# Performance work log

Measured on AMD Instinct MI355X. Metric: run time of the kernel, lower is better.

Reference implementation:

```python
import jax, jax.numpy as jnp
import numpy as np

B = 4096
N_DENSE = 13
N_SPARSE = 26
FEAT_PER_SPARSE = 1000
FIELD_NUM = N_DENSE + N_SPARSE          # 39
FEATURE_NUM = N_DENSE + N_SPARSE * FEAT_PER_SPARSE  # 26013
K = 16


def setup_inputs() -> dict:
    key = jax.random.key(0)
    k1, k2, k3, k4 = jax.random.split(key, 4)
    dense_inputs = jax.random.normal(k1, (B, N_DENSE), dtype=jnp.float32)
    sparse_inputs = jax.random.randint(k2, (B, N_SPARSE), 0, FEAT_PER_SPARSE, dtype=jnp.int32)
    w0 = jnp.zeros((1,), dtype=jnp.float32)
    w = jax.random.normal(k3, (FEATURE_NUM, 1), dtype=jnp.float32) * 0.05
    v = jax.random.normal(k4, (FEATURE_NUM, FIELD_NUM, K), dtype=jnp.float32) * 0.05
    return {"dense_inputs": dense_inputs, "sparse_inputs": sparse_inputs,
            "w0": w0, "w": w, "v": v}


def reference(dense_inputs, sparse_inputs, w0, w, v):
    # Feature-index layout matches tf.concat([dense cols, one_hot(sparse_0), ...]):
    # rows [0, N_DENSE) of w/v belong to dense fields, then FEAT_PER_SPARSE rows per sparse field.
    offsets = N_DENSE + FEAT_PER_SPARSE * jnp.arange(N_SPARSE, dtype=sparse_inputs.dtype)
    idx = sparse_inputs + offsets[None, :]               # [B, n_sparse] global feature ids

    # First order: w0 + onehot_concat @ w  ==  w0 + dense part + gathered sparse rows
    first_order = (w0
                   + dense_inputs @ w[:N_DENSE]                       # [B, 1]
                   + jnp.sum(w[idx, 0], axis=1, keepdims=True))       # [B, 1]

    # field_f = tensordot(onehot_concat, v) -> [B, field_num, k]
    field_f = (jnp.einsum('bd,dfk->bfk', dense_inputs, v[:N_DENSE])
               + jnp.sum(v[idx], axis=1))                             # [B, F, K]

    # sum_{i<j} <f_i, f_j> = 0.5 * (||sum_i f_i||^2 - sum_i ||f_i||^2)  (FM identity)
    s = jnp.sum(field_f, axis=1)                                      # [B, K]
    second_order = 0.5 * (jnp.sum(s * s, axis=-1)
                          - jnp.sum(field_f * field_f, axis=(1, 2)))  # [B]
    return first_order + second_order[:, None]
```

## Files before the change

### kernel.cpp

```cpp
#include <hip/hip_runtime.h>

#define NDENSE 13
#define NSPARSE 26
#define FIELD_NUM 39
#define KDIM 16
#define ROW_F4 156
#define BATCH 4096

__global__ __launch_bounds__(256) void ffm_kernel(
    const float* __restrict__ dense,
    const int*   __restrict__ sparse,
    const float* __restrict__ w0,
    const float* __restrict__ w,
    const float4* __restrict__ v4,
    float* __restrict__ out)
{
    const int wave = threadIdx.x >> 6;
    const int lane = threadIdx.x & 63;
    const int b = blockIdx.x * 4 + wave;

    float dv[NDENSE];
#pragma unroll
    for (int d = 0; d < NDENSE; ++d) dv[d] = dense[b * NDENSE + d];

    int myidx = 0;
    if (lane < NSPARSE) {
        myidx = sparse[b * NSPARSE + lane] + NDENSE + 1000 * lane;
    }

    float4 s = make_float4(0.f, 0.f, 0.f, 0.f);
    float  sq = 0.f;

#pragma unroll
    for (int p = 0; p < 3; ++p) {
        const int e4 = lane + 64 * p;
        if (e4 < ROW_F4) {
            float4 acc = make_float4(0.f, 0.f, 0.f, 0.f);
#pragma unroll
            for (int d = 0; d < NDENSE; ++d) {
                const float4 vv = v4[d * ROW_F4 + e4];
                acc.x += dv[d] * vv.x; acc.y += dv[d] * vv.y;
                acc.z += dv[d] * vv.z; acc.w += dv[d] * vv.w;
            }
#pragma unroll
            for (int j = 0; j < NSPARSE; ++j) {
                const int ij = __shfl(myidx, j);
                const float4 vv = v4[ij * ROW_F4 + e4];
                acc.x += vv.x; acc.y += vv.y; acc.z += vv.z; acc.w += vv.w;
            }
            s.x += acc.x; s.y += acc.y; s.z += acc.z; s.w += acc.w;
            sq  += acc.x * acc.x + acc.y * acc.y + acc.z * acc.z + acc.w * acc.w;
        }
    }

#pragma unroll
    for (int m = 4; m <= 32; m <<= 1) {
        s.x += __shfl_xor(s.x, m);
        s.y += __shfl_xor(s.y, m);
        s.z += __shfl_xor(s.z, m);
        s.w += __shfl_xor(s.w, m);
    }
    float s2 = s.x * s.x + s.y * s.y + s.z * s.z + s.w * s.w;
    s2 += __shfl_xor(s2, 1);
    s2 += __shfl_xor(s2, 2);

#pragma unroll
    for (int m = 1; m <= 32; m <<= 1) sq += __shfl_xor(sq, m);

    float fo = 0.f;
    if (lane < NSPARSE) fo = w[myidx];
    if (lane < NDENSE)  fo += dense[b * NDENSE + lane] * w[lane];
#pragma unroll
    for (int m = 1; m <= 32; m <<= 1) fo += __shfl_xor(fo, m);

    if (lane == 0) {
        out[b] = w0[0] + fo + 0.5f * (s2 - sq);
    }
}

extern "C" void kernel_launch(void* const* d_in, const int* in_sizes, int n_in,
                              void* d_out, int out_size, void* d_ws, size_t ws_size,
                              hipStream_t stream) {
    const float*  dense  = (const float*)d_in[0];
    const int*    sparse = (const int*)d_in[1];
    const float*  w0     = (const float*)d_in[2];
    const float*  w      = (const float*)d_in[3];
    const float4* v4     = (const float4*)d_in[4];
    float* out = (float*)d_out;

    dim3 grid(BATCH / 4);
    dim3 block(256);
    hipLaunchKernelGGL(ffm_kernel, grid, block, 0, stream,
                       dense, sparse, w0, w, v4, out);
}
```

Baseline: 43.66 us.

## Split dense projection into separate LDS-tiled GEMM kernel feeding gather kernel

Moves the dense-feature contraction against the first 13 rows of v into its own kernel. That kernel stages those rows in shared memory and writes a per-sample [156 float4] partial to workspace. The gather kernel then loads this precomputed partial instead of doing 13 global loads and FMAs per element. The cost is an extra launch plus a roughly 10 MB workspace write and read, and the fused kernel is kept as a fallback when workspace is too small.

```diff
diff --git a/kernel.cpp b/kernel.cpp
--- a/kernel.cpp
+++ b/kernel.cpp
@@ -2,31 +2,60 @@
 
 #define NDENSE 13
 #define NSPARSE 26
-#define FIELD_NUM 39
-#define KDIM 16
 #define ROW_F4 156
 #define BATCH 4096
+#define GEMM_ROWS 64
 
-__global__ __launch_bounds__(256) void ffm_kernel(
-    const float* __restrict__ dense,
-    const int*   __restrict__ sparse,
-    const float* __restrict__ w0,
-    const float* __restrict__ w,
+__global__ __launch_bounds__(256) void dense_gemm(
+    const float*  __restrict__ dense,
     const float4* __restrict__ v4,
-    float* __restrict__ out)
+    float4*       __restrict__ dv_out)
+{
+    __shared__ float4 vsh[NDENSE * ROW_F4];
+    __shared__ float  dsh[GEMM_ROWS * NDENSE];
+
+    const int t = threadIdx.x;
+    for (int i = t; i < NDENSE * ROW_F4; i += 256) vsh[i] = v4[i];
+    const int row0 = blockIdx.x * GEMM_ROWS;
+    for (int i = t; i < GEMM_ROWS * NDENSE; i += 256)
+        dsh[i] = dense[row0 * NDENSE + i];
+    __syncthreads();
+
+    const int r  = t >> 2;
+    const int c0 = t & 3;
+    float dl[NDENSE];
+#pragma unroll
+    for (int d = 0; d < NDENSE; ++d) dl[d] = dsh[r * NDENSE + d];
+
+#pragma unroll 4
+    for (int i = 0; i < ROW_F4 / 4; ++i) {
+        const int e = c0 + 4 * i;
+        float4 acc = make_float4(0.f, 0.f, 0.f, 0.f);
+#pragma unroll
+        for (int d = 0; d < NDENSE; ++d) {
+            const float4 vv = vsh[d * ROW_F4 + e];
+            acc.x += dl[d] * vv.x; acc.y += dl[d] * vv.y;
+            acc.z += dl[d] * vv.z; acc.w += dl[d] * vv.w;
+        }
+        dv_out[(size_t)(row0 + r) * ROW_F4 + e] = acc;
+    }
+}
+
+__global__ __launch_bounds__(256) void ffm_gather(
+    const float*  __restrict__ dense,
+    const int*    __restrict__ sparse,
+    const float*  __restrict__ w0,
+    const float*  __restrict__ w,
+    const float4* __restrict__ v4,
+    const float4* __restrict__ dvp,
+    float*        __restrict__ out)
 {
     const int wave = threadIdx.x >> 6;
     const int lane = threadIdx.x & 63;
     const int b = blockIdx.x * 4 + wave;
 
-    float dv[NDENSE];
-#pragma unroll
-    for (int d = 0; d < NDENSE; ++d) dv[d] = dense[b * NDENSE + d];
-
     int myidx = 0;
-    if (lane < NSPARSE) {
-        myidx = sparse[b * NSPARSE + lane] + NDENSE + 1000 * lane;
-    }
+    if (lane < NSPARSE) myidx = sparse[b * NSPARSE + lane] + NDENSE + 1000 * lane;
 
     float4 s = make_float4(0.f, 0.f, 0.f, 0.f);
     float  sq = 0.f;
@@ -35,17 +64,11 @@
     for (int p = 0; p < 3; ++p) {
         const int e4 = lane + 64 * p;
         if (e4 < ROW_F4) {
-            float4 acc = make_float4(0.f, 0.f, 0.f, 0.f);
-#pragma unroll
-            for (int d = 0; d < NDENSE; ++d) {
-                const float4 vv = v4[d * ROW_F4 + e4];
-                acc.x += dv[d] * vv.x; acc.y += dv[d] * vv.y;
-                acc.z += dv[d] * vv.z; acc.w += dv[d] * vv.w;
-            }
+            float4 acc = dvp[(size_t)b * ROW_F4 + e4];
 #pragma unroll
             for (int j = 0; j < NSPARSE; ++j) {
                 const int ij = __shfl(myidx, j);
-                const float4 vv = v4[ij * ROW_F4 + e4];
+                const float4 vv = v4[(size_t)ij * ROW_F4 + e4];
                 acc.x += vv.x; acc.y += vv.y; acc.z += vv.z; acc.w += vv.w;
             }
             s.x += acc.x; s.y += acc.y; s.z += acc.z; s.w += acc.w;
@@ -73,9 +96,64 @@
 #pragma unroll
     for (int m = 1; m <= 32; m <<= 1) fo += __shfl_xor(fo, m);
 
-    if (lane == 0) {
-        out[b] = w0[0] + fo + 0.5f * (s2 - sq);
+    if (lane == 0) out[b] = w0[0] + fo + 0.5f * (s2 - sq);
+}
+
+__global__ __launch_bounds__(256) void ffm_fused(
+    const float* __restrict__ dense, const int* __restrict__ sparse,
+    const float* __restrict__ w0, const float* __restrict__ w,
+    const float4* __restrict__ v4, float* __restrict__ out)
+{
+    const int wave = threadIdx.x >> 6;
+    const int lane = threadIdx.x & 63;
+    const int b = blockIdx.x * 4 + wave;
+
+    float dv[NDENSE];
+#pragma unroll
+    for (int d = 0; d < NDENSE; ++d) dv[d] = dense[b * NDENSE + d];
+
+    int myidx = 0;
+    if (lane < NSPARSE) myidx = sparse[b * NSPARSE + lane] + NDENSE + 1000 * lane;
+
+    float4 s = make_float4(0.f, 0.f, 0.f, 0.f);
+    float  sq = 0.f;
+#pragma unroll
+    for (int p = 0; p < 3; ++p) {
+        const int e4 = lane + 64 * p;
+        if (e4 < ROW_F4) {
+            float4 acc = make_float4(0.f, 0.f, 0.f, 0.f);
+#pragma unroll
+            for (int d = 0; d < NDENSE; ++d) {
+                const float4 vv = v4[d * ROW_F4 + e4];
+                acc.x += dv[d] * vv.x; acc.y += dv[d] * vv.y;
+                acc.z += dv[d] * vv.z; acc.w += dv[d] * vv.w;
+            }
+#pragma unroll
+            for (int j = 0; j < NSPARSE; ++j) {
+                const int ij = __shfl(myidx, j);
+                const float4 vv = v4[(size_t)ij * ROW_F4 + e4];
+                acc.x += vv.x; acc.y += vv.y; acc.z += vv.z; acc.w += vv.w;
+            }
+            s.x += acc.x; s.y += acc.y; s.z += acc.z; s.w += acc.w;
+            sq  += acc.x * acc.x + acc.y * acc.y + acc.z * acc.z + acc.w * acc.w;
+        }
     }
+#pragma unroll
+    for (int m = 4; m <= 32; m <<= 1) {
+        s.x += __shfl_xor(s.x, m); s.y += __shfl_xor(s.y, m);
+        s.z += __shfl_xor(s.z, m); s.w += __shfl_xor(s.w, m);
+    }
+    float s2 = s.x * s.x + s.y * s.y + s.z * s.z + s.w * s.w;
+    s2 += __shfl_xor(s2, 1);
+    s2 += __shfl_xor(s2, 2);
+#pragma unroll
+    for (int m = 1; m <= 32; m <<= 1) sq += __shfl_xor(sq, m);
+    float fo = 0.f;
+    if (lane < NSPARSE) fo = w[myidx];
+    if (lane < NDENSE)  fo += dense[b * NDENSE + lane] * w[lane];
+#pragma unroll
+    for (int m = 1; m <= 32; m <<= 1) fo += __shfl_xor(fo, m);
+    if (lane == 0) out[b] = w0[0] + fo + 0.5f * (s2 - sq);
 }
 
 extern "C" void kernel_launch(void* const* d_in, const int* in_sizes, int n_in,
@@ -88,8 +166,16 @@
     const float4* v4     = (const float4*)d_in[4];
     float* out = (float*)d_out;
 
-    dim3 grid(BATCH / 4);
-    dim3 block(256);
-    hipLaunchKernelGGL(ffm_kernel, grid, block, 0, stream,
-                       dense, sparse, w0, w, v4, out);
+    const size_t dv_bytes = (size_t)BATCH * ROW_F4 * sizeof(float4);
+
+    if (ws_size >= dv_bytes) {
+        float4* dvp = (float4*)d_ws;
+        hipLaunchKernelGGL(dense_gemm, dim3(BATCH / GEMM_ROWS), dim3(256), 0, stream,
+                           dense, v4, dvp);
+        hipLaunchKernelGGL(ffm_gather, dim3(BATCH / 4), dim3(256), 0, stream,
+                           dense, sparse, w0, w, v4, dvp, out);
+    } else {
+        hipLaunchKernelGGL(ffm_fused, dim3(BATCH / 4), dim3(256), 0, stream,
+                           dense, sparse, w0, w, v4, out);
+    }
 }
```

After: 58.39 us. 33.7% more time.

## Quantize FFM embedding table to fp8 and split into prep, square-sum and output kernels

Applied to the files above, without the earlier changes.

A prep kernel converts the whole v table to packed fp8. It also stores per-row exact field sums and a per-row norm-correction term. A sliced gather kernel then accumulates per-field vectors from the fp8 table to get squared norms, and a final kernel builds the sum-of-fields term from the exact row sums. The aim is to cut gather bandwidth to a quarter, at the cost of a full-table pass every call and fp8 rounding error in the cross terms, which the norm correction does not fully remove. A fused fp32 path is kept as a fallback when the workspace is too small.

```diff
diff --git a/kernel.cpp b/kernel.cpp
--- a/kernel.cpp
+++ b/kernel.cpp
@@ -2,35 +2,229 @@
 
 #define NDENSE 13
 #define NSPARSE 26
-#define FIELD_NUM 39
-#define KDIM 16
 #define ROW_F4 156
 #define BATCH 4096
-
-__global__ __launch_bounds__(256) void ffm_kernel(
+#define VROWS 26013
+#define ROW_U32 160
+#define ROW_U4  40
+#define NSLICE 10
+#define SRPB   64
+
+#if defined(__has_builtin)
+#if __has_builtin(__builtin_amdgcn_cvt_pk_fp8_f32) && __has_builtin(__builtin_amdgcn_cvt_pk_f32_fp8)
+#define FP8_HW 1
+#endif
+#endif
+
+typedef float f32x2 __attribute__((ext_vector_type(2)));
+
+__device__ inline unsigned enc1(float f) {
+    unsigned u = __float_as_uint(f);
+    unsigned s = (u >> 24) & 0x80u;
+    unsigned a = u & 0x7fffffffu;
+    if (a >= 0x3c800000u) {
+        unsigned r = a + 0x7ffffu + ((a >> 20) & 1u);
+        return s | ((r - (120u << 23)) >> 20);
+    }
+    return s | (unsigned)__float2uint_rn(__uint_as_float(a) * 512.f);
+}
+__device__ inline float dec1(unsigned b) {
+    unsigned em = b & 0x7fu;
+    float mag = (em >= 8u) ? __uint_as_float((em << 20) + (120u << 23))
+                           : (float)em * 0x1p-9f;
+    return (b & 0x80u) ? -mag : mag;
+}
+__device__ inline unsigned enc4(float4 x) {
+#ifdef FP8_HW
+    int pk = 0;
+    pk = __builtin_amdgcn_cvt_pk_fp8_f32(x.x, x.y, pk, false);
+    pk = __builtin_amdgcn_cvt_pk_fp8_f32(x.z, x.w, pk, true);
+    return (unsigned)pk;
+#else
+    return enc1(x.x) | (enc1(x.y) << 8) | (enc1(x.z) << 16) | (enc1(x.w) << 24);
+#endif
+}
+__device__ inline float4 dec4(unsigned p) {
+#ifdef FP8_HW
+    f32x2 lo = __builtin_amdgcn_cvt_pk_f32_fp8((int)p, false);
+    f32x2 hi = __builtin_amdgcn_cvt_pk_f32_fp8((int)p, true);
+    return make_float4(lo.x, lo.y, hi.x, hi.y);
+#else
+    return make_float4(dec1(p & 0xffu), dec1((p >> 8) & 0xffu),
+                       dec1((p >> 16) & 0xffu), dec1((p >> 24) & 0xffu));
+#endif
+}
+
+__global__ __launch_bounds__(256) void ffm_prep(
+    const float4* __restrict__ v4, unsigned* __restrict__ vh,
+    float* __restrict__ u, float* __restrict__ nrmc)
+{
+    const int wv = threadIdx.x >> 6, lane = threadIdx.x & 63;
+    const int row = blockIdx.x * 4 + wv;
+    if (row >= VROWS) return;
+
+    float4 us = make_float4(0.f, 0.f, 0.f, 0.f);
+    float  nc = 0.f;
+#pragma unroll
+    for (int p = 0; p < 3; ++p) {
+        const int e4 = lane + 64 * p;
+        if (e4 < ROW_F4) {
+            const float4 x = v4[(size_t)row * ROW_F4 + e4];
+            const unsigned pk = enc4(x);
+            const float4 xh = dec4(pk);
+            vh[(size_t)row * ROW_U32 + e4] = pk;
+            us.x += x.x; us.y += x.y; us.z += x.z; us.w += x.w;
+            nc += (x.x*x.x - xh.x*xh.x) + (x.y*x.y - xh.y*xh.y)
+                + (x.z*x.z - xh.z*xh.z) + (x.w*x.w - xh.w*xh.w);
+        } else if (e4 < ROW_U32) {
+            vh[(size_t)row * ROW_U32 + e4] = 0u;
+        }
+    }
+#pragma unroll
+    for (int m = 4; m <= 32; m <<= 1) {
+        us.x += __shfl_xor(us.x, m); us.y += __shfl_xor(us.y, m);
+        us.z += __shfl_xor(us.z, m); us.w += __shfl_xor(us.w, m);
+    }
+    if (lane < 4)
+        ((float4*)(u + (size_t)row * 16))[lane] = us;
+#pragma unroll
+    for (int m = 1; m <= 32; m <<= 1) nc += __shfl_xor(nc, m);
+    if (lane == 0) nrmc[row] = nc;
+}
+
+__global__ __launch_bounds__(256) void ffm_sq(
+    const float* __restrict__ dense,
+    const int*   __restrict__ sparse,
+    const float* __restrict__ v,
+    const uint4* __restrict__ vh4,
+    float*       __restrict__ part)
+{
+    const int x = blockIdx.x & 7;
+    const int i = blockIdx.x >> 3;
+    const int fid = x * 80 + i;
+    const int slice = fid >> 6, chunk = fid & 63;
+    const int row0 = chunk * SRPB;
+
+    __shared__ int    vrow_s[SRPB * NSPARSE];
+    __shared__ float  dsh   [SRPB * NDENSE];
+    __shared__ float4 vsh4  [NDENSE * 16];
+
+    const int t = threadIdx.x;
+    for (int q = t; q < SRPB * NSPARSE; q += 256) {
+        const int r = q / NSPARSE, j = q % NSPARSE;
+        vrow_s[q] = sparse[(row0 + r) * NSPARSE + j] + NDENSE + 1000 * j;
+    }
+    for (int q = t; q < SRPB * NDENSE; q += 256)
+        dsh[q] = dense[row0 * NDENSE + q];
+    for (int q = t; q < NDENSE * 64; q += 256) {
+        const int d = q >> 6, h = q & 63, col = slice * 64 + h;
+        ((float*)vsh4)[q] = (col < 624) ? v[(size_t)d * 624 + col] : 0.f;
+    }
+    __syncthreads();
+
+    const int lane = t & 63, wv = t >> 6;
+    const int rl = wv * 16 + (lane >> 2);
+    const int c  = lane & 3;
+
+    float4 av0 = make_float4(0.f,0.f,0.f,0.f), av1 = av0, av2 = av0, av3 = av0;
+
+#pragma unroll
+    for (int d = 0; d < NDENSE; ++d) {
+        const float wg = dsh[rl * NDENSE + d];
+        const float4 b0 = vsh4[d * 16 + c * 4 + 0];
+        const float4 b1 = vsh4[d * 16 + c * 4 + 1];
+        const float4 b2 = vsh4[d * 16 + c * 4 + 2];
+        const float4 b3 = vsh4[d * 16 + c * 4 + 3];
+        av0.x += wg*b0.x; av0.y += wg*b0.y; av0.z += wg*b0.z; av0.w += wg*b0.w;
+        av1.x += wg*b1.x; av1.y += wg*b1.y; av1.z += wg*b1.z; av1.w += wg*b1.w;
+        av2.x += wg*b2.x; av2.y += wg*b2.y; av2.z += wg*b2.z; av2.w += wg*b2.w;
+        av3.x += wg*b3.x; av3.y += wg*b3.y; av3.z += wg*b3.z; av3.w += wg*b3.w;
+    }
+
+#pragma unroll
+    for (int j = 0; j < NSPARSE; ++j) {
+        const unsigned r = (unsigned)vrow_s[rl * NSPARSE + j];
+        const uint4 g = vh4[(size_t)r * ROW_U4 + slice * 4 + c];
+        float4 d0 = dec4(g.x), d1 = dec4(g.y), d2 = dec4(g.z), d3 = dec4(g.w);
+        av0.x += d0.x; av0.y += d0.y; av0.z += d0.z; av0.w += d0.w;
+        av1.x += d1.x; av1.y += d1.y; av1.z += d1.z; av1.w += d1.w;
+        av2.x += d2.x; av2.y += d2.y; av2.z += d2.z; av2.w += d2.w;
+        av3.x += d3.x; av3.y += d3.y; av3.z += d3.z; av3.w += d3.w;
+    }
+
+    float sq = av0.x*av0.x + av0.y*av0.y + av0.z*av0.z + av0.w*av0.w
+             + av1.x*av1.x + av1.y*av1.y + av1.z*av1.z + av1.w*av1.w
+             + av2.x*av2.x + av2.y*av2.y + av2.z*av2.z + av2.w*av2.w
+             + av3.x*av3.x + av3.y*av3.y + av3.z*av3.z + av3.w*av3.w;
+    sq += __shfl_xor(sq, 1);
+    sq += __shfl_xor(sq, 2);
+    if (c == 0) part[slice * BATCH + row0 + rl] = sq;
+}
+
+__global__ __launch_bounds__(256) void ffm_out(
     const float* __restrict__ dense,
     const int*   __restrict__ sparse,
     const float* __restrict__ w0,
     const float* __restrict__ w,
-    const float4* __restrict__ v4,
-    float* __restrict__ out)
+    const float* __restrict__ u,
+    const float* __restrict__ nrmc,
+    const float* __restrict__ part,
+    float*       __restrict__ out)
 {
     const int wave = threadIdx.x >> 6;
     const int lane = threadIdx.x & 63;
     const int b = blockIdx.x * 4 + wave;
+    const int g = lane >> 4, k = lane & 15;
+
+    float s = 0.f;
+    for (int j = g; j < NSPARSE; j += 4) {
+        const int r = sparse[b * NSPARSE + j] + NDENSE + 1000 * j;
+        s += u[(size_t)r * 16 + k];
+    }
+    for (int d = g; d < NDENSE; d += 4)
+        s += dense[b * NDENSE + d] * u[(size_t)d * 16 + k];
+    s += __shfl_xor(s, 16);
+    s += __shfl_xor(s, 32);
+
+    float s2 = s * s;
+    s2 += __shfl_xor(s2, 1);
+    s2 += __shfl_xor(s2, 2);
+    s2 += __shfl_xor(s2, 4);
+    s2 += __shfl_xor(s2, 8);
+
+    float red = 0.f, fo = 0.f;
+    if (lane < NSLICE) red = part[lane * BATCH + b];
+    if (lane < NSPARSE) {
+        const int r = sparse[b * NSPARSE + lane] + NDENSE + 1000 * lane;
+        fo = w[r];
+        red += nrmc[r];
+    }
+    if (lane < NDENSE) fo += dense[b * NDENSE + lane] * w[lane];
+#pragma unroll
+    for (int m = 1; m <= 32; m <<= 1) {
+        fo  += __shfl_xor(fo, m);
+        red += __shfl_xor(red, m);
+    }
+    if (lane == 0) out[b] = w0[0] + fo + 0.5f * (s2 - red);
+}
+
+__global__ __launch_bounds__(256) void ffm_fused(
+    const float* __restrict__ dense, const int* __restrict__ sparse,
+    const float* __restrict__ w0, const float* __restrict__ w,
+    const float4* __restrict__ v4, float* __restrict__ out)
+{
+    const int wave = threadIdx.x >> 6;
+    const int lane = threadIdx.x & 63;
+    const int b = blockIdx.x * 4 + wave;
 
     float dv[NDENSE];
 #pragma unroll
     for (int d = 0; d < NDENSE; ++d) dv[d] = dense[b * NDENSE + d];
-
     int myidx = 0;
-    if (lane < NSPARSE) {
-        myidx = sparse[b * NSPARSE + lane] + NDENSE + 1000 * lane;
-    }
+    if (lane < NSPARSE) myidx = sparse[b * NSPARSE + lane] + NDENSE + 1000 * lane;
 
     float4 s = make_float4(0.f, 0.f, 0.f, 0.f);
     float  sq = 0.f;
-
 #pragma unroll
     for (int p = 0; p < 3; ++p) {
         const int e4 = lane + 64 * p;
@@ -39,43 +233,35 @@
 #pragma unroll
             for (int d = 0; d < NDENSE; ++d) {
                 const float4 vv = v4[d * ROW_F4 + e4];
-                acc.x += dv[d] * vv.x; acc.y += dv[d] * vv.y;
-                acc.z += dv[d] * vv.z; acc.w += dv[d] * vv.w;
+                acc.x += dv[d]*vv.x; acc.y += dv[d]*vv.y;
+                acc.z += dv[d]*vv.z; acc.w += dv[d]*vv.w;
             }
 #pragma unroll
             for (int j = 0; j < NSPARSE; ++j) {
                 const int ij = __shfl(myidx, j);
-                const float4 vv = v4[ij * ROW_F4 + e4];
+                const float4 vv = v4[(size_t)ij * ROW_F4 + e4];
                 acc.x += vv.x; acc.y += vv.y; acc.z += vv.z; acc.w += vv.w;
             }
             s.x += acc.x; s.y += acc.y; s.z += acc.z; s.w += acc.w;
-            sq  += acc.x * acc.x + acc.y * acc.y + acc.z * acc.z + acc.w * acc.w;
+            sq  += acc.x*acc.x + acc.y*acc.y + acc.z*acc.z + acc.w*acc.w;
         }
     }
-
 #pragma unroll
     for (int m = 4; m <= 32; m <<= 1) {
-        s.x += __shfl_xor(s.x, m);
-        s.y += __shfl_xor(s.y, m);
-        s.z += __shfl_xor(s.z, m);
-        s.w += __shfl_xor(s.w, m);
-    }
-    float s2 = s.x * s.x + s.y * s.y + s.z * s.z + s.w * s.w;
+        s.x += __shfl_xor(s.x, m); s.y += __shfl_xor(s.y, m);
+        s.z += __shfl_xor(s.z, m); s.w += __shfl_xor(s.w, m);
+    }
+    float s2 = s.x*s.x + s.y*s.y + s.z*s.z + s.w*s.w;
     s2 += __shfl_xor(s2, 1);
     s2 += __shfl_xor(s2, 2);
-
 #pragma unroll
     for (int m = 1; m <= 32; m <<= 1) sq += __shfl_xor(sq, m);
-
     float fo = 0.f;
     if (lane < NSPARSE) fo = w[myidx];
     if (lane < NDENSE)  fo += dense[b * NDENSE + lane] * w[lane];
 #pragma unroll
     for (int m = 1; m <= 32; m <<= 1) fo += __shfl_xor(fo, m);
-
-    if (lane == 0) {
-        out[b] = w0[0] + fo + 0.5f * (s2 - sq);
-    }
+    if (lane == 0) out[b] = w0[0] + fo + 0.5f * (s2 - sq);
 }
 
 extern "C" void kernel_launch(void* const* d_in, const int* in_sizes, int n_in,
@@ -85,11 +271,32 @@
     const int*    sparse = (const int*)d_in[1];
     const float*  w0     = (const float*)d_in[2];
     const float*  w      = (const float*)d_in[3];
+    const float*  v      = (const float*)d_in[4];
     const float4* v4     = (const float4*)d_in[4];
     float* out = (float*)d_out;
 
-    dim3 grid(BATCH / 4);
-    dim3 block(256);
-    hipLaunchKernelGGL(ffm_kernel, grid, block, 0, stream,
-                       dense, sparse, w0, w, v4, out);
-}
+    const size_t VH_B   = (size_t)VROWS * 640;
+    const size_t U_OFF  = (VH_B + 255) & ~(size_t)255;
+    const size_t U_B    = (size_t)VROWS * 16 * 4;
+    const size_t NC_OFF = (U_OFF + U_B + 255) & ~(size_t)255;
+    const size_t NC_B   = (size_t)VROWS * 4;
+    const size_t PT_OFF = (NC_OFF + NC_B + 255) & ~(size_t)255;
+    const size_t PT_B   = (size_t)NSLICE * BATCH * 4;
+
+    if (ws_size >= PT_OFF + PT_B) {
+        unsigned* vh  = (unsigned*)d_ws;
+        float*    u   = (float*)((char*)d_ws + U_OFF);
+        float*    nc  = (float*)((char*)d_ws + NC_OFF);
+        float*    prt = (float*)((char*)d_ws + PT_OFF);
+
+        hipLaunchKernelGGL(ffm_prep, dim3((VROWS + 3) / 4), dim3(256), 0, stream,
+                           v4, vh, u, nc);
+        hipLaunchKernelGGL(ffm_sq, dim3(8 * 80), dim3(256), 0, stream,
+                           dense, sparse, v, (const uint4*)vh, prt);
+        hipLaunchKernelGGL(ffm_out, dim3(BATCH / 4), dim3(256), 0, stream,
+                           dense, sparse, w0, w, u, nc, prt, out);
+    } else {
+        hipLaunchKernelGGL(ffm_fused, dim3(BATCH / 4), dim3(256), 0, stream,
+                           dense, sparse, w0, w, v4, out);
+    }
+}
```

Measured after the change: 40.28 us. 1.08x faster.
